# Performance work log

Hardware: AMD Instinct MI355X
Metric: run time of the kernel (lower is better)

## Reference

```python
import jax, jax.numpy as jnp
import numpy as np

N = 10000          # num nodes
E = 160000         # num edges (avg degree 16)
F = 128            # num_features
S = 4              # num_species
RAD = 8            # radial_embedding_dim
RO = 16            # readout_mlp_irreps = 16x0e
EPS = 0.17677669529663687  # epsilon = 1/sqrt(avg_degree)
ACT_NORM = 1.679177        # normalize_function(silu): 1/sqrt(E[silu(x)^2]), x~N(0,1)


def nsilu(x):
    return jax.nn.silu(x) * ACT_NORM


def setup_inputs() -> dict:
    key = jax.random.key(0)
    ks = jax.random.split(key, 24)
    d = {}
    d["vectors"] = jax.random.normal(ks[0], (E, 3), jnp.float32)
    d["node_scalars"] = jax.random.normal(ks[1], (N, F), jnp.float32)
    d["node_vectors"] = jax.random.normal(ks[2], (N, F, 3), jnp.float32)
    d["radial_embeddings"] = jax.random.normal(ks[3], (E, RAD), jnp.float32)
    # linear_up (irrep-wise linear on 0e and 1o)
    d["W_up_s"] = jax.random.normal(ks[4], (F, F), jnp.float32)
    d["W_up_v"] = jax.random.normal(ks[5], (F, F), jnp.float32)
    # radial MLP [RAD,64,64,64,weight_dim=4F]
    d["W_mlp1"] = jax.random.normal(ks[6], (RAD, 64), jnp.float32) / np.sqrt(RAD)
    d["b_mlp1"] = jnp.zeros((64,), jnp.float32)
    d["W_mlp2"] = jax.random.normal(ks[7], (64, 64), jnp.float32) / np.sqrt(64.0)
    d["b_mlp2"] = jnp.zeros((64,), jnp.float32)
    d["W_mlp3"] = jax.random.normal(ks[8], (64, 64), jnp.float32) / np.sqrt(64.0)
    d["b_mlp3"] = jnp.zeros((64,), jnp.float32)
    d["W_mlp4"] = jax.random.normal(ks[9], (64, 4 * F), jnp.float32) / np.sqrt(64.0)
    d["b_mlp4"] = jnp.zeros((4 * F,), jnp.float32)
    # linear_down: TP out (2F x 0e + 2F x 1o) -> F x (0e+1o)
    d["W_down_s"] = jax.random.normal(ks[10], (2 * F, F), jnp.float32)
    d["W_down_v"] = jax.random.normal(ks[11], (2 * F, F), jnp.float32)
    # species-indexed skip linear (output is hidden_out = 0e only, since last=True)
    d["Wz_s"] = jax.random.normal(ks[12], (S, F, F), jnp.float32)
    # symmetric contraction weights: 5 invariant basis terms per channel per species
    d["W_sc"] = jax.random.normal(ks[13], (S, 5, F), jnp.float32)
    d["W_post"] = jax.random.normal(ks[14], (F, F), jnp.float32)
    d["W_ro1"] = jax.random.normal(ks[15], (F, RO), jnp.float32)
    d["W_ro2"] = jax.random.normal(ks[16], (RO, 1), jnp.float32)
    d["senders"] = jax.random.randint(ks[17], (E,), 0, N)
    d["receivers"] = jax.random.randint(ks[18], (E,), 0, N)
    d["num_species_counts"] = jnp.full((S,), N // S, dtype=jnp.int32)
    d["num_nodes"] = N
    return d


def reference(vectors, node_scalars, node_vectors, radial_embeddings,
              W_up_s, W_up_v,
              W_mlp1, b_mlp1, W_mlp2, b_mlp2, W_mlp3, b_mlp3, W_mlp4, b_mlp4,
              W_down_s, W_down_v, Wz_s, W_sc, W_post, W_ro1, W_ro2,
              senders, receivers, num_species_counts, num_nodes):
    # spherical harmonics (max_ell=1): Y0 = 1, Y1 = unit edge vector
    rnorm = jnp.linalg.norm(vectors, axis=-1, keepdims=True)
    Y1 = vectors / (rnorm + 1e-12)                      # [E,3]

    # species index per node from counts
    i = jnp.repeat(jnp.arange(S), num_species_counts, total_repeat_length=num_nodes)

    # self connection (species-indexed linear on input scalars; hidden_out = 0e)
    self_conn = jnp.einsum('nf,nfg->ng', node_scalars, Wz_s[i]) / np.sqrt(F)

    # linear_up (irrep-wise)
    s = node_scalars @ W_up_s / np.sqrt(F)              # [N,F]
    v = jnp.einsum('nfc,fg->ngc', node_vectors, W_up_v) / np.sqrt(F)  # [N,F,3]

    # radial MLP -> per-edge channelwise TP weights, 4 paths x F channels
    h = nsilu(radial_embeddings @ W_mlp1 + b_mlp1)
    h = nsilu(h @ W_mlp2 + b_mlp2)
    h = nsilu(h @ W_mlp3 + b_mlp3)
    mix = (h @ W_mlp4 + b_mlp4).reshape(-1, 4, F)       # [E,4,F]

    # channelwise tensor product: gather sender feats, combine with sph
    sg = s[senders]                                     # [E,F]
    vg = v[senders]                                     # [E,F,3]
    m_s0 = mix[:, 0] * sg                               # 0e x 0e -> 0e
    m_s3 = mix[:, 3] * (jnp.einsum('efc,ec->ef', vg, Y1) / np.sqrt(3.0))  # 1o x 1o -> 0e
    m_v1 = mix[:, 1][..., None] * sg[..., None] * Y1[:, None, :]          # 0e x 1o -> 1o
    m_v2 = mix[:, 2][..., None] * vg                                      # 1o x 0e -> 1o
    msg_s = jnp.concatenate([m_s0, m_s3], axis=-1)      # [E,2F]
    msg_v = jnp.concatenate([m_v1, m_v2], axis=1)       # [E,2F,3]

    # scatter to receivers
    agg_s = jax.ops.segment_sum(msg_s, receivers, num_segments=num_nodes) * EPS
    agg_v = jax.ops.segment_sum(msg_v, receivers, num_segments=num_nodes) * EPS

    # linear_down: 2F -> F per irrep
    s2 = agg_s @ W_down_s / np.sqrt(2 * F)              # [N,F]
    v2 = jnp.einsum('nfc,fg->ngc', agg_v, W_down_v) / np.sqrt(2 * F)  # [N,F,3]

    # symmetric contraction (correlation<=3, output 0e): per-species weighted
    # invariant basis {s, s^2, |v|^2, s^3, s|v|^2} per channel
    vv = jnp.sum(v2 * v2, axis=-1)                      # [N,F]
    basis = jnp.stack([s2, s2 * s2, vv, s2 * s2 * s2, s2 * vv], axis=1)  # [N,5,F]
    sc = jnp.sum(W_sc[i] * basis, axis=1)               # [N,F]

    feats = sc @ W_post / np.sqrt(F) + self_conn        # [N,F]

    # readout (last=True): linear -> scalar activation -> linear
    hr = nsilu(feats @ W_ro1 / np.sqrt(F))              # [N,16]
    node_outputs = hr @ W_ro2 / np.sqrt(RO)             # [N,1]
    return (node_outputs, feats)
```

## Files before the change

kernel.cpp:

```cpp
#include <hip/hip_runtime.h>
#include <hip/hip_bf16.h>
#include <math.h>

#define N_NODES 10000
#define N_EDGES 160000
#define F 128
#define TE 128
#define HS 72

typedef _Float16 v8h __attribute__((ext_vector_type(8)));
typedef _Float16 v4h __attribute__((ext_vector_type(4)));
typedef float    v4f __attribute__((ext_vector_type(4)));

__device__ __forceinline__ float nsilu(float x) {
    return 1.679177f * (x / (1.0f + expf(-x)));
}

__device__ __forceinline__ void fma4(float4& a, float s, const float4& b) {
    a.x = fmaf(s, b.x, a.x); a.y = fmaf(s, b.y, a.y);
    a.z = fmaf(s, b.z, a.z); a.w = fmaf(s, b.w, a.w);
}

__device__ __forceinline__ int species_of(int n, const int* __restrict__ counts) {
    int c0 = counts[0];
    int c01 = c0 + counts[1];
    int c012 = c01 + counts[2];
    return (n >= c0) + (n >= c01) + (n >= c012);
}

__global__ __launch_bounds__(256) void k_setup(
    const int* __restrict__ receivers, int* __restrict__ deg,
    const float* __restrict__ W2, const float* __restrict__ W3,
    const float* __restrict__ W4, const float* __restrict__ b4,
    const float* __restrict__ Wup_s, const float* __restrict__ Wup_v,
    const float* __restrict__ Wz, const float* __restrict__ Wds,
    const float* __restrict__ Wdv, const float* __restrict__ Wpost,
    _Float16* __restrict__ W2t, _Float16* __restrict__ W3t,
    _Float16* __restrict__ W4t, float* __restrict__ b4p,
    _Float16* __restrict__ Wup_s_t, _Float16* __restrict__ Wup_v_t,
    _Float16* __restrict__ Wz_t, _Float16* __restrict__ Wds_t,
    _Float16* __restrict__ Wdv_t, _Float16* __restrict__ Wpost_t,
    const float* __restrict__ ns, const float* __restrict__ nv,
    _Float16* __restrict__ ns16, _Float16* __restrict__ nv16)
{
    int gidx = blockIdx.x * 256 + threadIdx.x;
    if (gidx < N_EDGES) {
        atomicAdd(&deg[receivers[gidx]], 1);
        return;
    }
    int idx = gidx - N_EDGES;
    if (idx < 221696) {
        if (idx < 4096) {
            int u = idx >> 6, k = idx & 63;
            W2t[idx] = (_Float16)W2[k * 64 + u];
        } else if (idx < 8192) {
            int j = idx - 4096;
            int u = j >> 6, k = j & 63;
            W3t[j] = (_Float16)W3[k * 64 + u];
        } else if (idx < 40960) {
            int j = idx - 8192;
            int gn = j >> 6, k = j & 63;
            int go = (gn & 3) * 128 + (gn >> 2);
            W4t[j] = (_Float16)W4[k * 512 + go];
        } else if (idx < 41472) {
            int j = idx - 40960;
            int go = (j & 3) * 128 + (j >> 2);
            b4p[j] = b4[go];
        } else if (idx < 57856) {
            int j = idx - 41472;
            int g = j >> 7, f = j & 127;
            Wup_s_t[j] = (_Float16)Wup_s[f * 128 + g];
        } else if (idx < 74240) {
            int j = idx - 57856;
            int g = j >> 7, f = j & 127;
            Wup_v_t[j] = (_Float16)Wup_v[f * 128 + g];
        } else if (idx < 139776) {
            int j = idx - 74240;
            int s = j >> 14, r = j & 16383;
            int g = r >> 7, f = r & 127;
            Wz_t[j] = (_Float16)Wz[s * 16384 + f * 128 + g];
        } else if (idx < 172544) {
            int j = idx - 139776;
            int g = j >> 8, k = j & 255;
            Wds_t[j] = (_Float16)Wds[k * 128 + g];
        } else if (idx < 205312) {
            int j = idx - 172544;
            int g = j >> 8, k = j & 255;
            Wdv_t[j] = (_Float16)Wdv[k * 128 + g];
        } else {
            int j = idx - 205312;
            int g = j >> 7, f = j & 127;
            Wpost_t[j] = (_Float16)Wpost[f * 128 + g];
        }
        return;
    }
    int j = idx - 221696;
    if (j < N_NODES * F) {
        ns16[j] = (_Float16)ns[j];
    } else if (j < 4 * N_NODES * F) {
        int j2 = j - N_NODES * F;
        int row = j2 >> 7, f = j2 & 127;
        int n = row / 3, c = row - n * 3;
        nv16[j2] = (_Float16)nv[((size_t)n * F + f) * 3 + c];
    }
}

__global__ __launch_bounds__(1024) void k_scan(const int* __restrict__ deg,
                                               int* __restrict__ offs,
                                               int* __restrict__ cursor) {
    __shared__ int sums[1024];
    const int t = threadIdx.x;
    const int CH = 10;
    int base = t * CH;
    int local[CH];
    int s = 0;
    #pragma unroll
    for (int j = 0; j < CH; ++j) {
        int v = (base + j < N_NODES) ? deg[base + j] : 0;
        local[j] = s;
        s += v;
    }
    sums[t] = s;
    __syncthreads();
    for (int off = 1; off < 1024; off <<= 1) {
        int v = (t >= off) ? sums[t - off] : 0;
        __syncthreads();
        sums[t] += v;
        __syncthreads();
    }
    int carry = (t == 0) ? 0 : sums[t - 1];
    #pragma unroll
    for (int j = 0; j < CH; ++j) {
        int idx = base + j;
        if (idx < N_NODES) {
            int o = carry + local[j];
            offs[idx] = o;
            cursor[idx] = o;
        }
    }
    if (t == 1023) offs[N_NODES] = sums[1023];
}

__global__ __launch_bounds__(256) void k_fill(const int* __restrict__ receivers,
                                              const int* __restrict__ senders,
                                              const float* __restrict__ vectors,
                                              const float* __restrict__ radial,
                                              int* __restrict__ cursor,
                                              float4* __restrict__ yq,
                                              float4* __restrict__ re_csr) {
    int e = blockIdx.x * 256 + threadIdx.x;
    if (e < N_EDGES) {
        int pos = atomicAdd(&cursor[receivers[e]], 1);
        float vx = vectors[e * 3 + 0];
        float vy = vectors[e * 3 + 1];
        float vz = vectors[e * 3 + 2];
        float inv = 1.0f / (sqrtf(vx * vx + vy * vy + vz * vz) + 1e-12f);
        float4 y;
        y.x = vx * inv; y.y = vy * inv; y.z = vz * inv;
        y.w = __int_as_float(senders[e]);
        yq[pos] = y;
        const float4* rp = (const float4*)(radial + (size_t)e * 8);
        re_csr[pos * 2]     = rp[0];
        re_csr[pos * 2 + 1] = rp[1];
    }
}

template <int K, typename OT>
__device__ __forceinline__ void gemm_tile(
    const _Float16* __restrict__ A, const _Float16* __restrict__ Bg,
    OT* __restrict__ out, int M, int row0, float scale,
    _Float16* Bl, const int* __restrict__ counts, int sp)
{
    const int t = threadIdx.x;
    constexpr int KP = K + 8;
    __syncthreads();
    for (int idx = t; idx < 128 * (K / 8); idx += 256) {
        int g = idx / (K / 8), kk = (idx % (K / 8)) * 8;
        *(v8h*)(Bl + g * KP + kk) = *(const v8h*)(Bg + g * K + kk);
    }
    __syncthreads();

    const int lane = t & 63;
    const int w = t >> 6;
    const int c = lane & 15;
    const int q = lane >> 4;

    v4f acc[2][8];
    #pragma unroll
    for (int mi = 0; mi < 2; ++mi)
        #pragma unroll
        for (int nt = 0; nt < 8; ++nt)
            acc[mi][nt] = (v4f){0.f, 0.f, 0.f, 0.f};

    for (int ch = 0; ch < K / 32; ++ch) {
        v8h a[2];
        #pragma unroll
        for (int mi = 0; mi < 2; ++mi) {
            int r = row0 + (2 * w + mi) * 16 + c;
            r = min(r, M - 1);
            a[mi] = *(const v8h*)(A + (size_t)r * K + ch * 32 + q * 8);
        }
        #pragma unroll
        for (int nt = 0; nt < 8; ++nt) {
            v8h b = *(const v8h*)(Bl + (nt * 16 + c) * KP + ch * 32 + q * 8);
            acc[0][nt] = __builtin_amdgcn_mfma_f32_16x16x32_f16(a[0], b, acc[0][nt], 0, 0, 0);
            acc[1][nt] = __builtin_amdgcn_mfma_f32_16x16x32_f16(a[1], b, acc[1][nt], 0, 0, 0);
        }
    }
    #pragma unroll
    for (int mi = 0; mi < 2; ++mi) {
        #pragma unroll
        for (int r = 0; r < 4; ++r) {
            int row = row0 + (2 * w + mi) * 16 + q * 4 + r;
            bool ok = row < M;
            if (ok && sp >= 0) ok = (species_of(row, counts) == sp);
            if (ok) {
                OT* op = out + (size_t)row * 128;
                #pragma unroll
                for (int nt = 0; nt < 8; ++nt)
                    op[nt * 16 + c] = (OT)(acc[mi][nt][r] * scale);
            }
        }
    }
}

__global__ __launch_bounds__(256) void k_gemm_up(
    const _Float16* __restrict__ ns16, const _Float16* __restrict__ nv16,
    const _Float16* __restrict__ Wup_s_t, const _Float16* __restrict__ Wup_v_t,
    const _Float16* __restrict__ Wz_t, const int* __restrict__ counts,
    _Float16* __restrict__ s16, _Float16* __restrict__ v16,
    float* __restrict__ selfc)
{
    __shared__ _Float16 Bl[128 * 136];
    const int row0 = blockIdx.x * 128;
    const float isf = 0.08838834764831845f;
    if (blockIdx.y == 0) {
        if (row0 >= N_NODES) return;
        gemm_tile<128, _Float16>(ns16, Wup_s_t, s16, N_NODES, row0, isf, Bl, counts, -1);
    } else if (blockIdx.y == 1) {
        gemm_tile<128, _Float16>(nv16, Wup_v_t, v16, 3 * N_NODES, row0, isf, Bl, counts, -1);
    } else {
        if (row0 >= N_NODES) return;
        int sp0 = species_of(row0, counts);
        int sp1 = species_of(min(row0 + 127, N_NODES - 1), counts);
        for (int sp = sp0; sp <= sp1; ++sp)
            gemm_tile<128, float>(ns16, Wz_t + (size_t)sp * 16384, selfc,
                                  N_NODES, row0, isf, Bl, counts, sp);
    }
}

__global__ __launch_bounds__(256) void k_gemm_down(
    const _Float16* __restrict__ agg_s16, const _Float16* __restrict__ agg_v16,
    const _Float16* __restrict__ Wds_t, const _Float16* __restrict__ Wdv_t,
    const int* __restrict__ counts,
    float* __restrict__ s2, float* __restrict__ v2)
{
    __shared__ _Float16 Bl[128 * 264];
    const int row0 = blockIdx.x * 128;
    if (blockIdx.y == 0) {
        if (row0 >= N_NODES) return;
        gemm_tile<256, float>(agg_s16, Wds_t, s2, N_NODES, row0, 1.0f, Bl, counts, -1);
    } else {
        gemm_tile<256, float>(agg_v16, Wdv_t, v2, 3 * N_NODES, row0, 1.0f, Bl, counts, -1);
    }
}

__device__ __forceinline__ void mfma_layer64(
    const _Float16* src, _Float16* dst,
    const _Float16* __restrict__ Wt, const float* __restrict__ b,
    int w, int q, int c)
{
    v8h B[4][2];
    float bias[4];
    #pragma unroll
    for (int nt = 0; nt < 4; ++nt) {
        B[nt][0] = *(const v8h*)(Wt + (nt * 16 + c) * 64 + q * 8);
        B[nt][1] = *(const v8h*)(Wt + (nt * 16 + c) * 64 + 32 + q * 8);
        bias[nt] = b[nt * 16 + c];
    }
    #pragma unroll
    for (int mi = 0; mi < 2; ++mi) {
        int mt = 2 * w + mi;
        v8h a0 = *(const v8h*)(src + (mt * 16 + c) * HS + q * 8);
        v8h a1 = *(const v8h*)(src + (mt * 16 + c) * HS + 32 + q * 8);
        #pragma unroll
        for (int nt = 0; nt < 4; ++nt) {
            v4f acc = {bias[nt], bias[nt], bias[nt], bias[nt]};
            acc = __builtin_amdgcn_mfma_f32_16x16x32_f16(a0, B[nt][0], acc, 0, 0, 0);
            acc = __builtin_amdgcn_mfma_f32_16x16x32_f16(a1, B[nt][1], acc, 0, 0, 0);
            #pragma unroll
            for (int r = 0; r < 4; ++r)
                dst[(mt * 16 + q * 4 + r) * HS + nt * 16 + c] = (_Float16)nsilu(acc[r]);
        }
    }
}

__global__ __launch_bounds__(256) void k_mlp(
    const float* __restrict__ re_csr,
    const float* __restrict__ W1, const float* __restrict__ b1,
    const _Float16* __restrict__ W2t, const float* __restrict__ b2,
    const _Float16* __restrict__ W3t, const float* __restrict__ b3,
    const _Float16* __restrict__ W4t, const float* __restrict__ b4p,
    _Float16* __restrict__ mix)
{
    __shared__ float sre[TE * 8];
    __shared__ _Float16 hA[TE * HS];
    __shared__ _Float16 hB[TE * HS];

    const int t = threadIdx.x;
    const int p0 = blockIdx.x * TE;

    ((float4*)sre)[t] = ((const float4*)(re_csr + (size_t)p0 * 8))[t];
    __syncthreads();

    {
        const int uslot = t & 15;
        const int egrp = t >> 4;
        const int u0 = uslot * 4;
        float4 w[8];
        #pragma unroll
        for (int k = 0; k < 8; ++k) w[k] = *(const float4*)(W1 + k * 64 + u0);
        float4 bb = *(const float4*)(b1 + u0);
        #pragma unroll
        for (int i = 0; i < 8; ++i) {
            int e = egrp + i * 16;
            const float* rp = sre + e * 8;
            float4 a = bb;
            #pragma unroll
            for (int k = 0; k < 8; ++k) fma4(a, rp[k], w[k]);
            v4h r = {(_Float16)nsilu(a.x), (_Float16)nsilu(a.y),
                     (_Float16)nsilu(a.z), (_Float16)nsilu(a.w)};
            *(v4h*)(hA + e * HS + u0) = r;
        }
    }
    __syncthreads();

    const int lane = t & 63;
    const int w = t >> 6;
    const int c = lane & 15;
    const int q = lane >> 4;

    mfma_layer64(hA, hB, W2t, b2, w, q, c);
    mfma_layer64(hB, hA, W3t, b3, w, q, c);
    __syncthreads();

    v8h B4[8][2];
    float bias4[8];
    #pragma unroll
    for (int j = 0; j < 8; ++j) {
        int g = (8 * w + j) * 16 + c;
        B4[j][0] = *(const v8h*)(W4t + g * 64 + q * 8);
        B4[j][1] = *(const v8h*)(W4t + g * 64 + 32 + q * 8);
        bias4[j] = b4p[g];
    }
    for (int mt = 0; mt < 8; ++mt) {
        v8h a0 = *(const v8h*)(hA + (mt * 16 + c) * HS + q * 8);
        v8h a1 = *(const v8h*)(hA + (mt * 16 + c) * HS + 32 + q * 8);
        size_t rowbase = (size_t)(p0 + mt * 16 + q * 4) * 512;
        #pragma unroll
        for (int j = 0; j < 8; ++j) {
            v4f acc = {bias4[j], bias4[j], bias4[j], bias4[j]};
            acc = __builtin_amdgcn_mfma_f32_16x16x32_f16(a0, B4[j][0], acc, 0, 0, 0);
            acc = __builtin_amdgcn_mfma_f32_16x16x32_f16(a1, B4[j][1], acc, 0, 0, 0);
            int gcol = (8 * w + j) * 16 + c;
            #pragma unroll
            for (int r = 0; r < 4; ++r)
                mix[rowbase + (size_t)r * 512 + gcol] = (_Float16)acc[r];
        }
    }
}

__global__ __launch_bounds__(128) void k_gather(
    const _Float16* __restrict__ mix, const float4* __restrict__ yq,
    const _Float16* __restrict__ s16, const _Float16* __restrict__ v16,
    const int* __restrict__ offs,
    _Float16* __restrict__ agg_s16, _Float16* __restrict__ agg_v16)
{
    const int n = blockIdx.x;
    const int f = threadIdx.x;
    const int beg = offs[n], end = offs[n + 1];
    const float inv_sqrt3 = 0.5773502691896258f;
    __shared__ float4 ly[32];

    float as0 = 0, as1 = 0;
    float av00 = 0, av01 = 0, av02 = 0, av10 = 0, av11 = 0, av12 = 0;

    for (int c0 = beg; c0 < end; c0 += 32) {
        int cnt = min(32, end - c0);
        __syncthreads();
        if (f < cnt) ly[f] = yq[c0 + f];
        __syncthreads();
        #pragma unroll 4
        for (int i = 0; i < cnt; ++i) {
            float4 y = ly[i];
            int snd = __float_as_int(y.w);

            union { uint2 u; _Float16 h[4]; } mu;
            mu.u = *(const uint2*)(mix + (size_t)(c0 + i) * 512 + f * 4);
            float m0 = (float)mu.h[0];
            float m1 = (float)mu.h[1];
            float m2 = (float)mu.h[2];
            float m3 = (float)mu.h[3];

            float sg = (float)s16[(size_t)snd * F + f];
            const _Float16* vb = v16 + (size_t)snd * 384;
            float vg0 = (float)vb[f];
            float vg1 = (float)vb[128 + f];
            float vg2 = (float)vb[256 + f];

            as0 += m0 * sg;
            as1 += m3 * (vg0 * y.x + vg1 * y.y + vg2 * y.z) * inv_sqrt3;
            float w1s = m1 * sg;
            av00 += w1s * y.x; av01 += w1s * y.y; av02 += w1s * y.z;
            av10 += m2 * vg0;  av11 += m2 * vg1;  av12 += m2 * vg2;
        }
    }
    const float SC = 0.011048543456039804f;
    agg_s16[(size_t)n * 256 + f]       = (_Float16)(as0 * SC);
    agg_s16[(size_t)n * 256 + 128 + f] = (_Float16)(as1 * SC);
    _Float16* av = agg_v16 + (size_t)n * 768;
    av[0 * 256 + f]       = (_Float16)(av00 * SC);
    av[0 * 256 + 128 + f] = (_Float16)(av10 * SC);
    av[1 * 256 + f]       = (_Float16)(av01 * SC);
    av[1 * 256 + 128 + f] = (_Float16)(av11 * SC);
    av[2 * 256 + f]       = (_Float16)(av02 * SC);
    av[2 * 256 + 128 + f] = (_Float16)(av12 * SC);
}

__global__ __launch_bounds__(256) void k_contract(
    const float* __restrict__ s2, const float* __restrict__ v2,
    const float* __restrict__ Wsc, const int* __restrict__ counts,
    _Float16* __restrict__ sc16)
{
    int idx = blockIdx.x * 256 + threadIdx.x;
    int n = idx >> 7, g = idx & 127;
    float s = s2[idx];
    const float* vp = v2 + (size_t)n * 384;
    float a0 = vp[g], a1 = vp[128 + g], a2 = vp[256 + g];
    float vv = a0 * a0 + a1 * a1 + a2 * a2;
    const float* w = Wsc + (size_t)species_of(n, counts) * 640;
    float sc = w[g] * s + w[128 + g] * (s * s) + w[256 + g] * vv
             + w[384 + g] * (s * s * s) + w[512 + g] * (s * vv);
    sc16[idx] = (_Float16)sc;
}

__global__ __launch_bounds__(256) void k_post(
    const _Float16* __restrict__ sc16, const _Float16* __restrict__ Wpost_t,
    const float* __restrict__ selfc,
    const float* __restrict__ Wro1, const float* __restrict__ Wro2,
    float* __restrict__ out)
{
    __shared__ _Float16 Bl[128 * 136];
    __shared__ float sfeat[128][132];
    __shared__ float shr[128][16];
    const int t = threadIdx.x;
    const int row0 = blockIdx.x * 128;
    const float isf = 0.08838834764831845f;

    for (int idx = t; idx < 128 * 16; idx += 256) {
        int g = idx >> 4, kk = (idx & 15) * 8;
        *(v8h*)(Bl + g * 136 + kk) = *(const v8h*)(Wpost_t + g * 128 + kk);
    }
    __syncthreads();

    const int lane = t & 63;
    const int w = t >> 6;
    const int c = lane & 15;
    const int q = lane >> 4;

    v4f acc[2][8];
    #pragma unroll
    for (int mi = 0; mi < 2; ++mi)
        #pragma unroll
        for (int nt = 0; nt < 8; ++nt)
            acc[mi][nt] = (v4f){0.f, 0.f, 0.f, 0.f};

    for (int ch = 0; ch < 4; ++ch) {
        v8h a[2];
        #pragma unroll
        for (int mi = 0; mi < 2; ++mi) {
            int r = row0 + (2 * w + mi) * 16 + c;
            r = min(r, N_NODES - 1);
            a[mi] = *(const v8h*)(sc16 + (size_t)r * 128 + ch * 32 + q * 8);
        }
        #pragma unroll
        for (int nt = 0; nt < 8; ++nt) {
            v8h b = *(const v8h*)(Bl + (nt * 16 + c) * 136 + ch * 32 + q * 8);
            acc[0][nt] = __builtin_amdgcn_mfma_f32_16x16x32_f16(a[0], b, acc[0][nt], 0, 0, 0);
            acc[1][nt] = __builtin_amdgcn_mfma_f32_16x16x32_f16(a[1], b, acc[1][nt], 0, 0, 0);
        }
    }
    #pragma unroll
    for (int mi = 0; mi < 2; ++mi) {
        #pragma unroll
        for (int r = 0; r < 4; ++r) {
            int row = row0 + (2 * w + mi) * 16 + q * 4 + r;
            int rl = (2 * w + mi) * 16 + q * 4 + r;
            if (row < N_NODES) {
                #pragma unroll
                for (int nt = 0; nt < 8; ++nt) {
                    int col = nt * 16 + c;
                    float feat = acc[mi][nt][r] * isf + selfc[(size_t)row * 128 + col];
                    out[N_NODES + (size_t)row * 128 + col] = feat;
                    sfeat[rl][col] = feat;
                }
            } else {
                #pragma unroll
                for (int nt = 0; nt < 8; ++nt) sfeat[rl][nt * 16 + c] = 0.f;
            }
        }
    }
    __syncthreads();

    for (int idx = t; idx < 2048; idx += 256) {
        int nd = idx >> 4, u = idx & 15;
        float a = 0;
        for (int f = 0; f < 128; f += 4) {
            float4 x = *(const float4*)&sfeat[nd][f];
            a += x.x * Wro1[(f + 0) * 16 + u] + x.y * Wro1[(f + 1) * 16 + u]
               + x.z * Wro1[(f + 2) * 16 + u] + x.w * Wro1[(f + 3) * 16 + u];
        }
        shr[nd][u] = nsilu(a * isf);
    }
    __syncthreads();

    if (t < 128 && row0 + t < N_NODES) {
        float a = 0;
        #pragma unroll
        for (int j = 0; j < 16; ++j) a += shr[t][j] * Wro2[j];
        out[row0 + t] = a * 0.25f;
    }
}


extern "C" void kernel_launch(void* const* d_in, const int* in_sizes, int n_in,
                              void* d_out, int out_size, void* d_ws, size_t ws_size,
                              hipStream_t stream) {
    const float* vectors      = (const float*)d_in[0];
    const float* node_scalars = (const float*)d_in[1];
    const float* node_vectors = (const float*)d_in[2];
    const float* radial       = (const float*)d_in[3];
    const float* W_up_s       = (const float*)d_in[4];
    const float* W_up_v       = (const float*)d_in[5];
    const float* W1 = (const float*)d_in[6];
    const float* b1 = (const float*)d_in[7];
    const float* W2 = (const float*)d_in[8];
    const float* b2 = (const float*)d_in[9];
    const float* W3 = (const float*)d_in[10];
    const float* b3 = (const float*)d_in[11];
    const float* W4 = (const float*)d_in[12];
    const float* b4 = (const float*)d_in[13];
    const float* Wds  = (const float*)d_in[14];
    const float* Wdv  = (const float*)d_in[15];
    const float* Wz   = (const float*)d_in[16];
    const float* Wsc  = (const float*)d_in[17];
    const float* Wpost= (const float*)d_in[18];
    const float* Wro1 = (const float*)d_in[19];
    const float* Wro2 = (const float*)d_in[20];
    const int* senders   = (const int*)d_in[21];
    const int* receivers = (const int*)d_in[22];
    const int* counts    = (const int*)d_in[23];
    float* out = (float*)d_out;

    const size_t NF = (size_t)N_NODES * F;

    char* base = (char*)d_ws;
    _Float16* mix = (_Float16*)base;
    float* s2   = (float*)base;
    float* v2   = s2 + NF;
    _Float16* sc16 = (_Float16*)(v2 + 3 * NF);

    char* p = base + (size_t)N_EDGES * 512 * 2;
    float4* yq     = (float4*)p;          p += (size_t)N_EDGES * 16;
    _Float16* ns16 = (_Float16*)p;        p += NF * 2;
    _Float16* nv16 = (_Float16*)p;        p += 3 * NF * 2;
    _Float16* s16  = (_Float16*)p;        p += NF * 2;
    _Float16* v16  = (_Float16*)p;        p += 3 * NF * 2;
    float* selfc   = (float*)p;           p += NF * 4;
    _Float16* agg_s16 = (_Float16*)p;     p += 2 * NF * 2;
    _Float16* agg_v16 = (_Float16*)p;     p += 6 * NF * 2;
    int* deg    = (int*)p;                p += N_NODES * 4;
    int* offs   = (int*)p;                p += (N_NODES + 1) * 4 + 12;
    int* cursor = (int*)p;                p += N_NODES * 4;
    _Float16* W2t = (_Float16*)p;         p += 4096 * 2;
    _Float16* W3t = (_Float16*)p;         p += 4096 * 2;
    _Float16* W4t = (_Float16*)p;         p += 32768 * 2;
    float* b4p    = (float*)p;            p += 512 * 4;
    _Float16* Wup_s_t = (_Float16*)p;     p += 16384 * 2;
    _Float16* Wup_v_t = (_Float16*)p;     p += 16384 * 2;
    _Float16* Wz_t    = (_Float16*)p;     p += 65536 * 2;
    _Float16* Wds_t   = (_Float16*)p;     p += 32768 * 2;
    _Float16* Wdv_t   = (_Float16*)p;     p += 32768 * 2;
    _Float16* Wpost_t = (_Float16*)p;     p += 16384 * 2;

    float4* re_csr = (float4*)agg_v16;

    hipMemsetAsync(deg, 0, N_NODES * sizeof(int), stream);

    k_setup<<<21491, 256, 0, stream>>>(
        receivers, deg, W2, W3, W4, b4, W_up_s, W_up_v, Wz, Wds, Wdv, Wpost,
        W2t, W3t, W4t, b4p, Wup_s_t, Wup_v_t, Wz_t, Wds_t, Wdv_t, Wpost_t,
        node_scalars, node_vectors, ns16, nv16);

    k_scan<<<1, 1024, 0, stream>>>(deg, offs, cursor);

    k_fill<<<(N_EDGES + 255) / 256, 256, 0, stream>>>(
        receivers, senders, vectors, radial, cursor, yq, re_csr);

    k_gemm_up<<<dim3(235, 3), 256, 0, stream>>>(
        ns16, nv16, Wup_s_t, Wup_v_t, Wz_t, counts, s16, v16, selfc);

    k_mlp<<<N_EDGES / TE, 256, 0, stream>>>(
        (const float*)re_csr, W1, b1, W2t, b2, W3t, b3, W4t, b4p, mix);

    k_gather<<<N_NODES, 128, 0, stream>>>(
        mix, yq, s16, v16, offs, agg_s16, agg_v16);

    k_gemm_down<<<dim3(235, 2), 256, 0, stream>>>(
        agg_s16, agg_v16, Wds_t, Wdv_t, counts, s2, v2);

    k_contract<<<(N_NODES * F) / 256, 256, 0, stream>>>(s2, v2, Wsc, counts, sc16);

    k_post<<<(N_NODES + 127) / 128, 256, 0, stream>>>(
        sc16, Wpost_t, selfc, Wro1, Wro2, out);
}
```

Before: 304.1 us.

## Fuse contraction into post kernel, MFMA readout, transpose MLP output stores

The symmetric contraction kernel is folded into the post kernel, which computes the per-channel basis directly into shared memory instead of writing and re-reading an fp16 intermediate. The first readout linear now runs on MFMA, using a transposed fp16 copy of Wro1 prepared in setup, instead of a scalar fp32 loop. The final MLP layer swaps its MFMA operands so each lane writes four contiguous fp16 outputs as one vector store instead of four strided scalar stores. In exchange, the readout features are rounded to fp16 before the Wro1 product, and the post kernel's shared-memory use changes.

```diff
diff --git a/kernel.cpp b/kernel.cpp
--- a/kernel.cpp
+++ b/kernel.cpp
@@ -35,11 +35,13 @@
     const float* __restrict__ Wup_s, const float* __restrict__ Wup_v,
     const float* __restrict__ Wz, const float* __restrict__ Wds,
     const float* __restrict__ Wdv, const float* __restrict__ Wpost,
+    const float* __restrict__ Wro1,
     _Float16* __restrict__ W2t, _Float16* __restrict__ W3t,
     _Float16* __restrict__ W4t, float* __restrict__ b4p,
     _Float16* __restrict__ Wup_s_t, _Float16* __restrict__ Wup_v_t,
     _Float16* __restrict__ Wz_t, _Float16* __restrict__ Wds_t,
     _Float16* __restrict__ Wdv_t, _Float16* __restrict__ Wpost_t,
+    _Float16* __restrict__ Wro1t,
     const float* __restrict__ ns, const float* __restrict__ nv,
     _Float16* __restrict__ ns16, _Float16* __restrict__ nv16)
 {
@@ -49,7 +51,7 @@
         return;
     }
     int idx = gidx - N_EDGES;
-    if (idx < 221696) {
+    if (idx < 223744) {
         if (idx < 4096) {
             int u = idx >> 6, k = idx & 63;
             W2t[idx] = (_Float16)W2[k * 64 + u];
@@ -87,14 +89,18 @@
             int j = idx - 172544;
             int g = j >> 8, k = j & 255;
             Wdv_t[j] = (_Float16)Wdv[k * 128 + g];
-        } else {
+        } else if (idx < 221696) {
             int j = idx - 205312;
             int g = j >> 7, f = j & 127;
             Wpost_t[j] = (_Float16)Wpost[f * 128 + g];
+        } else {
+            int j = idx - 221696;
+            int u = j >> 7, f = j & 127;
+            Wro1t[j] = (_Float16)Wro1[f * 16 + u];
         }
         return;
     }
-    int j = idx - 221696;
+    int j = idx - 223744;
     if (j < N_NODES * F) {
         ns16[j] = (_Float16)ns[j];
     } else if (j < 4 * N_NODES * F) {
@@ -344,28 +350,28 @@
     mfma_layer64(hB, hA, W3t, b3, w, q, c);
     __syncthreads();
 
-    v8h B4[8][2];
-    float bias4[8];
+    v8h A4[8][2];
+    v4f bias4[8];
     #pragma unroll
     for (int j = 0; j < 8; ++j) {
-        int g = (8 * w + j) * 16 + c;
-        B4[j][0] = *(const v8h*)(W4t + g * 64 + q * 8);
-        B4[j][1] = *(const v8h*)(W4t + g * 64 + 32 + q * 8);
-        bias4[j] = b4p[g];
+        int g0 = (8 * w + j) * 16;
+        A4[j][0] = *(const v8h*)(W4t + (g0 + c) * 64 + q * 8);
+        A4[j][1] = *(const v8h*)(W4t + (g0 + c) * 64 + 32 + q * 8);
+        float4 bb = *(const float4*)(b4p + g0 + q * 4);
+        bias4[j] = (v4f){bb.x, bb.y, bb.z, bb.w};
     }
     for (int mt = 0; mt < 8; ++mt) {
-        v8h a0 = *(const v8h*)(hA + (mt * 16 + c) * HS + q * 8);
-        v8h a1 = *(const v8h*)(hA + (mt * 16 + c) * HS + 32 + q * 8);
-        size_t rowbase = (size_t)(p0 + mt * 16 + q * 4) * 512;
+        v8h h0 = *(const v8h*)(hA + (mt * 16 + c) * HS + q * 8);
+        v8h h1 = *(const v8h*)(hA + (mt * 16 + c) * HS + 32 + q * 8);
+        size_t rowbase = (size_t)(p0 + mt * 16 + c) * 512;
         #pragma unroll
         for (int j = 0; j < 8; ++j) {
-            v4f acc = {bias4[j], bias4[j], bias4[j], bias4[j]};
-            acc = __builtin_amdgcn_mfma_f32_16x16x32_f16(a0, B4[j][0], acc, 0, 0, 0);
-            acc = __builtin_amdgcn_mfma_f32_16x16x32_f16(a1, B4[j][1], acc, 0, 0, 0);
-            int gcol = (8 * w + j) * 16 + c;
-            #pragma unroll
-            for (int r = 0; r < 4; ++r)
-                mix[rowbase + (size_t)r * 512 + gcol] = (_Float16)acc[r];
+            v4f acc = bias4[j];
+            acc = __builtin_amdgcn_mfma_f32_16x16x32_f16(A4[j][0], h0, acc, 0, 0, 0);
+            acc = __builtin_amdgcn_mfma_f32_16x16x32_f16(A4[j][1], h1, acc, 0, 0, 0);
+            v4h r = {(_Float16)acc[0], (_Float16)acc[1],
+                     (_Float16)acc[2], (_Float16)acc[3]};
+            *(v4h*)(mix + rowbase + (8 * w + j) * 16 + q * 4) = r;
         }
     }
 }
@@ -427,32 +433,16 @@
     av[2 * 256 + 128 + f] = (_Float16)(av12 * SC);
 }
 
-__global__ __launch_bounds__(256) void k_contract(
+__global__ __launch_bounds__(256) void k_post(
     const float* __restrict__ s2, const float* __restrict__ v2,
     const float* __restrict__ Wsc, const int* __restrict__ counts,
-    _Float16* __restrict__ sc16)
-{
-    int idx = blockIdx.x * 256 + threadIdx.x;
-    int n = idx >> 7, g = idx & 127;
-    float s = s2[idx];
-    const float* vp = v2 + (size_t)n * 384;
-    float a0 = vp[g], a1 = vp[128 + g], a2 = vp[256 + g];
-    float vv = a0 * a0 + a1 * a1 + a2 * a2;
-    const float* w = Wsc + (size_t)species_of(n, counts) * 640;
-    float sc = w[g] * s + w[128 + g] * (s * s) + w[256 + g] * vv
-             + w[384 + g] * (s * s * s) + w[512 + g] * (s * vv);
-    sc16[idx] = (_Float16)sc;
-}
-
-__global__ __launch_bounds__(256) void k_post(
-    const _Float16* __restrict__ sc16, const _Float16* __restrict__ Wpost_t,
-    const float* __restrict__ selfc,
-    const float* __restrict__ Wro1, const float* __restrict__ Wro2,
+    const _Float16* __restrict__ Wpost_t, const float* __restrict__ selfc,
+    const _Float16* __restrict__ Wro1t, const float* __restrict__ Wro2,
     float* __restrict__ out)
 {
     __shared__ _Float16 Bl[128 * 136];
-    __shared__ float sfeat[128][132];
-    __shared__ float shr[128][16];
+    __shared__ _Float16 Al[128 * 136];
+    __shared__ float shr[128 * 16];
     const int t = threadIdx.x;
     const int row0 = blockIdx.x * 128;
     const float isf = 0.08838834764831845f;
@@ -460,6 +450,41 @@
     for (int idx = t; idx < 128 * 16; idx += 256) {
         int g = idx >> 4, kk = (idx & 15) * 8;
         *(v8h*)(Bl + g * 136 + kk) = *(const v8h*)(Wpost_t + g * 128 + kk);
+    }
+
+    #pragma unroll 4
+    for (int i = 0; i < 16; ++i) {
+        int idx = t + i * 256;
+        int r = idx >> 5, c4 = idx & 31;
+        int rc = min(row0 + r, N_NODES - 1);
+        float4 s4 = *(const float4*)(s2 + (size_t)rc * 128 + c4 * 4);
+        float4 a0 = *(const float4*)(v2 + ((size_t)rc * 3 + 0) * 128 + c4 * 4);
+        float4 a1 = *(const float4*)(v2 + ((size_t)rc * 3 + 1) * 128 + c4 * 4);
+        float4 a2 = *(const float4*)(v2 + ((size_t)rc * 3 + 2) * 128 + c4 * 4);
+        const float* w = Wsc + (size_t)species_of(rc, counts) * 640 + c4 * 4;
+        float4 w0 = *(const float4*)(w);
+        float4 w1 = *(const float4*)(w + 128);
+        float4 w2 = *(const float4*)(w + 256);
+        float4 w3 = *(const float4*)(w + 384);
+        float4 w4 = *(const float4*)(w + 512);
+        v4h r16;
+        {
+            float s = s4.x, vv = a0.x*a0.x + a1.x*a1.x + a2.x*a2.x;
+            r16[0] = (_Float16)(w0.x*s + w1.x*(s*s) + w2.x*vv + w3.x*(s*s*s) + w4.x*(s*vv));
+        }
+        {
+            float s = s4.y, vv = a0.y*a0.y + a1.y*a1.y + a2.y*a2.y;
+            r16[1] = (_Float16)(w0.y*s + w1.y*(s*s) + w2.y*vv + w3.y*(s*s*s) + w4.y*(s*vv));
+        }
+        {
+            float s = s4.z, vv = a0.z*a0.z + a1.z*a1.z + a2.z*a2.z;
+            r16[2] = (_Float16)(w0.z*s + w1.z*(s*s) + w2.z*vv + w3.z*(s*s*s) + w4.z*(s*vv));
+        }
+        {
+            float s = s4.w, vv = a0.w*a0.w + a1.w*a1.w + a2.w*a2.w;
+            r16[3] = (_Float16)(w0.w*s + w1.w*(s*s) + w2.w*vv + w3.w*(s*s*s) + w4.w*(s*vv));
+        }
+        *(v4h*)(Al + r * 136 + c4 * 4) = r16;
     }
     __syncthreads();
 
@@ -478,11 +503,8 @@
     for (int ch = 0; ch < 4; ++ch) {
         v8h a[2];
         #pragma unroll
-        for (int mi = 0; mi < 2; ++mi) {
-            int r = row0 + (2 * w + mi) * 16 + c;
-            r = min(r, N_NODES - 1);
-            a[mi] = *(const v8h*)(sc16 + (size_t)r * 128 + ch * 32 + q * 8);
-        }
+        for (int mi = 0; mi < 2; ++mi)
+            a[mi] = *(const v8h*)(Al + ((2 * w + mi) * 16 + c) * 136 + ch * 32 + q * 8);
         #pragma unroll
         for (int nt = 0; nt < 8; ++nt) {
             v8h b = *(const v8h*)(Bl + (nt * 16 + c) * 136 + ch * 32 + q * 8);
@@ -490,6 +512,8 @@
             acc[1][nt] = __builtin_amdgcn_mfma_f32_16x16x32_f16(a[1], b, acc[1][nt], 0, 0, 0);
         }
     }
+    __syncthreads();
+
     #pragma unroll
     for (int mi = 0; mi < 2; ++mi) {
         #pragma unroll
@@ -502,32 +526,40 @@
                     int col = nt * 16 + c;
                     float feat = acc[mi][nt][r] * isf + selfc[(size_t)row * 128 + col];
                     out[N_NODES + (size_t)row * 128 + col] = feat;
-                    sfeat[rl][col] = feat;
+                    Al[rl * 136 + col] = (_Float16)feat;
                 }
             } else {
                 #pragma unroll
-                for (int nt = 0; nt < 8; ++nt) sfeat[rl][nt * 16 + c] = 0.f;
+                for (int nt = 0; nt < 8; ++nt) Al[rl * 136 + nt * 16 + c] = (_Float16)0.f;
             }
         }
     }
     __syncthreads();
 
-    for (int idx = t; idx < 2048; idx += 256) {
-        int nd = idx >> 4, u = idx & 15;
-        float a = 0;
-        for (int f = 0; f < 128; f += 4) {
-            float4 x = *(const float4*)&sfeat[nd][f];
-            a += x.x * Wro1[(f + 0) * 16 + u] + x.y * Wro1[(f + 1) * 16 + u]
-               + x.z * Wro1[(f + 2) * 16 + u] + x.w * Wro1[(f + 3) * 16 + u];
-        }
-        shr[nd][u] = nsilu(a * isf);
-    }
+    v4f hacc[2];
+    hacc[0] = (v4f){0.f, 0.f, 0.f, 0.f};
+    hacc[1] = (v4f){0.f, 0.f, 0.f, 0.f};
+    for (int ch = 0; ch < 4; ++ch) {
+        v8h b = *(const v8h*)(Wro1t + c * 128 + ch * 32 + q * 8);
+        #pragma unroll
+        for (int mi = 0; mi < 2; ++mi) {
+            v8h a = *(const v8h*)(Al + ((2 * w + mi) * 16 + c) * 136 + ch * 32 + q * 8);
+            hacc[mi] = __builtin_amdgcn_mfma_f32_16x16x32_f16(a, b, hacc[mi], 0, 0, 0);
+        }
+    }
+    #pragma unroll
+    for (int mi = 0; mi < 2; ++mi)
+        #pragma unroll
+        for (int r = 0; r < 4; ++r) {
+            int rl = (2 * w + mi) * 16 + q * 4 + r;
+            shr[rl * 16 + c] = nsilu(hacc[mi][r] * isf);
+        }
     __syncthreads();
 
     if (t < 128 && row0 + t < N_NODES) {
         float a = 0;
         #pragma unroll
-        for (int j = 0; j < 16; ++j) a += shr[t][j] * Wro2[j];
+        for (int j = 0; j < 16; ++j) a += shr[t * 16 + j] * Wro2[j];
         out[row0 + t] = a * 0.25f;
     }
 }
@@ -568,7 +600,6 @@
     _Float16* mix = (_Float16*)base;
     float* s2   = (float*)base;
     float* v2   = s2 + NF;
-    _Float16* sc16 = (_Float16*)(v2 + 3 * NF);
 
     char* p = base + (size_t)N_EDGES * 512 * 2;
     float4* yq     = (float4*)p;          p += (size_t)N_EDGES * 16;
@@ -592,14 +623,15 @@
     _Float16* Wds_t   = (_Float16*)p;     p += 32768 * 2;
     _Float16* Wdv_t   = (_Float16*)p;     p += 32768 * 2;
     _Float16* Wpost_t = (_Float16*)p;     p += 16384 * 2;
+    _Float16* Wro1t   = (_Float16*)p;     p += 2048 * 2;
 
     float4* re_csr = (float4*)agg_v16;
 
     hipMemsetAsync(deg, 0, N_NODES * sizeof(int), stream);
 
-    k_setup<<<21491, 256, 0, stream>>>(
-        receivers, deg, W2, W3, W4, b4, W_up_s, W_up_v, Wz, Wds, Wdv, Wpost,
-        W2t, W3t, W4t, b4p, Wup_s_t, Wup_v_t, Wz_t, Wds_t, Wdv_t, Wpost_t,
+    k_setup<<<21499, 256, 0, stream>>>(
+        receivers, deg, W2, W3, W4, b4, W_up_s, W_up_v, Wz, Wds, Wdv, Wpost, Wro1,
+        W2t, W3t, W4t, b4p, Wup_s_t, Wup_v_t, Wz_t, Wds_t, Wdv_t, Wpost_t, Wro1t,
         node_scalars, node_vectors, ns16, nv16);
 
     k_scan<<<1, 1024, 0, stream>>>(deg, offs, cursor);
@@ -619,8 +651,6 @@
     k_gemm_down<<<dim3(235, 2), 256, 0, stream>>>(
         agg_s16, agg_v16, Wds_t, Wdv_t, counts, s2, v2);
 
-    k_contract<<<(N_NODES * F) / 256, 256, 0, stream>>>(s2, v2, Wsc, counts, sc16);
-
     k_post<<<(N_NODES + 127) / 128, 256, 0, stream>>>(
-        sc16, Wpost_t, selfc, Wro1, Wro2, out);
-}
+        s2, v2, Wsc, counts, Wpost_t, selfc, Wro1t, Wro2, out);
+}
```

New measurement: 315.3 us. +3.7%, slower.
